# Kernel optimization log

Hardware: AMD Instinct MI355X
Metric: run time of the kernel (lower is better)

## Reference

```python
import jax, jax.numpy as jnp
import numpy as np

B, N, F = 32, 64, 128   # batch, nodes, input features (F == hidden_dim)
E = N * (N - 1)         # fully-connected directed edges = 4032
H, D = 4, 64            # heads, out_dim per head
ALPHA = 0.2             # leaky relu slope


def setup_inputs() -> dict:
    key = jax.random.key(0)
    ks = jax.random.split(key, 16)
    v_self = jax.random.normal(ks[0], (B, N, F), dtype=jnp.float32)
    # fully-connected one-hot sender/receiver matrices [E, N], broadcast to [B, E, N]
    pairs = np.array([(i, j) for i in range(N) for j in range(N) if i != j])
    send = np.zeros((E, N), np.float32); send[np.arange(E), pairs[:, 0]] = 1.0
    rec = np.zeros((E, N), np.float32); rec[np.arange(E), pairs[:, 1]] = 1.0
    rel_send = jnp.broadcast_to(jnp.asarray(send), (B, E, N))
    rel_rec = jnp.broadcast_to(jnp.asarray(rec), (B, E, N))
    s = 0.05
    return {
        "v_self": v_self,
        "rel_rec": rel_rec,
        "rel_send": rel_send,
        "W_proj": jax.random.normal(ks[1], (H * D, F), dtype=jnp.float32) * s,
        "a_fwd": jax.random.normal(ks[2], (H, D), dtype=jnp.float32) * s,
        "a_bwd": jax.random.normal(ks[3], (H, D), dtype=jnp.float32) * s,
        "We1": jax.random.normal(ks[4], (D, 2 * D), dtype=jnp.float32) * s,
        "be1": jnp.zeros((D,), jnp.float32),
        "We2": jax.random.normal(ks[5], (D, D), dtype=jnp.float32) * s,
        "be2": jnp.zeros((D,), jnp.float32),
        "Wv1": jax.random.normal(ks[6], (F, D), dtype=jnp.float32) * s,
        "bv1": jnp.zeros((F,), jnp.float32),
        "Wv2": jax.random.normal(ks[7], (F, F), dtype=jnp.float32) * s,
        "bv2": jnp.zeros((F,), jnp.float32),
        "Wv3": jax.random.normal(ks[8], (D, F), dtype=jnp.float32) * s,
        "bv3": jnp.zeros((D,), jnp.float32),
    }


def _leaky(x):
    return jnp.where(x >= 0, x, ALPHA * x)


def reference(v_self, rel_rec, rel_send, W_proj, a_fwd, a_bwd,
              We1, be1, We2, be2, Wv1, bv1, Wv2, bv2, Wv3, bv3):
    # project: [B,N,F] -> [B,N,H,D]
    v_proj = (v_self @ W_proj.T).reshape(B, N, H, D)
    # gather to edges via one-hot adjacency (v_src==h_src, v_tgt==h_tgt in original)
    h_src = jnp.einsum('ben,bnhd->behd', rel_send, v_proj)
    h_tgt = jnp.einsum('ben,bnhd->behd', rel_rec, v_proj)
    attn_ij = _leaky(jnp.einsum('behd,hd->beh', h_src, a_fwd)) / 500.0
    attn_ji = _leaky(jnp.einsum('behd,hd->beh', h_tgt, a_bwd)) / 500.0
    attn_max = jnp.maximum(attn_ij, attn_ji)
    # NOTE: original applies exp twice (exp of exp); reproduced faithfully
    e_ij = jnp.exp(jnp.exp(attn_ij - attn_max))
    e_ji = jnp.exp(jnp.exp(attn_ji - attn_max))
    alpha_sum = e_ij + e_ji
    alpha_ij = e_ij / alpha_sum   # [B,E,H]
    alpha_ji = e_ji / alpha_sum
    edge_input = jnp.concatenate(
        [alpha_ij[..., None] * h_src, alpha_ji[..., None] * h_tgt], axis=-1)  # [B,E,H,2D]
    # f_CG_e: Linear(2D->D), ReLU, Linear(D->D) on last dim
    e_cg = jax.nn.relu(edge_input @ We1.T + be1) @ We2.T + be2
    edge_weighted = e_cg * alpha_ij[..., None]                               # [B,E,H,D]
    # scatter back to nodes
    v_social = jnp.einsum('behd,ben->bnhd', edge_weighted, rel_rec)          # [B,N,H,D]
    # f_CG_v: Linear(D->F), ReLU, Linear(F->F), ReLU, Linear(F->D)
    x = jax.nn.relu(v_social @ Wv1.T + bv1)
    x = jax.nn.relu(x @ Wv2.T + bv2)
    x = x @ Wv3.T + bv3
    v_out = x.reshape(B, N, H * D)  # concat_heads=True
    return (v_out, alpha_ij)
```

## Files before the change

kernel.cpp:

```cpp
#include <hip/hip_runtime.h>

#define B_ 32
#define N_ 64
#define F_ 128
#define E_ 4032
#define H_ 4
#define D_ 64

typedef __bf16 bf16x8 __attribute__((ext_vector_type(8)));
typedef __bf16 bf16x4 __attribute__((ext_vector_type(4)));
typedef float  f32x4  __attribute__((ext_vector_type(4)));

#define MFMA(a, b, c) __builtin_amdgcn_mfma_f32_16x16x32_bf16(a, b, c, 0, 0, 0)


static __device__ inline bf16x8 ld_cvt8(const float* __restrict__ p) {
    float4 w0 = *(const float4*)p, w1 = *(const float4*)(p + 4);
    bf16x8 b;
    b[0]=(__bf16)w0.x; b[1]=(__bf16)w0.y; b[2]=(__bf16)w0.z; b[3]=(__bf16)w0.w;
    b[4]=(__bf16)w1.x; b[5]=(__bf16)w1.y; b[6]=(__bf16)w1.z; b[7]=(__bf16)w1.w;
    return b;
}

__global__ __launch_bounds__(256) void k_proj(
    const float* __restrict__ v_self, const float* __restrict__ W_proj,
    const float* __restrict__ We1,
    const float* __restrict__ a_fwd, const float* __restrict__ a_bwd,
    const float* __restrict__ Wv1, const float* __restrict__ We2,
    const float* __restrict__ be2, const float* __restrict__ Wv2,
    const float* __restrict__ Wv3,
    float* __restrict__ s_fwd, float* __restrict__ s_bwd,
    __bf16* __restrict__ u_src, __bf16* __restrict__ u_tgt,
    __bf16* __restrict__ M1bf, float* __restrict__ wb,
    __bf16* __restrict__ Wv2bf, __bf16* __restrict__ Wv3bf)
{
    const int t = threadIdx.x;
    const int blk = blockIdx.x;

    if (blk < 32) {
        const int pid = blk * 256 + t;
        const int f = pid >> 6, k = pid & 63;
        float acc = 0.f;
#pragma unroll 8
        for (int dd = 0; dd < 64; ++dd)
            acc += Wv1[f * 64 + dd] * We2[dd * 64 + k];
        M1bf[pid] = (__bf16)acc;
        float p = Wv1[f * 64 + k] * be2[k];
#pragma unroll
        for (int m = 1; m < 64; m <<= 1) p += __shfl_xor(p, m);
        if (k == 0) wb[f] = p;
        Wv2bf[pid]        = (__bf16)Wv2[pid];
        Wv2bf[pid + 8192] = (__bf16)Wv2[pid + 8192];
        Wv3bf[pid]        = (__bf16)Wv3[pid];
        return;
    }

    const int bid = blk - 32;
    const int tile = bid >> 2, w = bid & 3;
    const int node0 = tile * 16;
    const int wsub = t >> 6;
    const int l = t & 63, q = l >> 4, lr = l & 15;

    __shared__ __bf16 P_lds[16 * 72];
    __shared__ float  spart_f[4][16], spart_b[4][16];

    f32x4 acc = {};
#pragma unroll
    for (int ks = 0; ks < 4; ++ks) {
        bf16x8 a = ld_cvt8(v_self + (size_t)(node0 + lr) * 128 + ks * 32 + q * 8);
        bf16x8 bb = ld_cvt8(W_proj + (size_t)(w * 64 + wsub * 16 + lr) * 128 + ks * 32 + q * 8);
        acc = MFMA(a, bb, acc);
    }

    {
        float af = a_fwd[w * 64 + wsub * 16 + lr];
        float ab = a_bwd[w * 64 + wsub * 16 + lr];
        float pf[4], pb[4];
#pragma unroll
        for (int r = 0; r < 4; ++r) { pf[r] = acc[r] * af; pb[r] = acc[r] * ab; }
#pragma unroll
        for (int m = 1; m < 16; m <<= 1)
#pragma unroll
            for (int r = 0; r < 4; ++r) { pf[r] += __shfl_xor(pf[r], m); pb[r] += __shfl_xor(pb[r], m); }
        if (lr == 0) {
#pragma unroll
            for (int r = 0; r < 4; ++r) {
                spart_f[wsub][q * 4 + r] = pf[r];
                spart_b[wsub][q * 4 + r] = pb[r];
            }
        }
#pragma unroll
        for (int r = 0; r < 4; ++r)
            P_lds[(q * 4 + r) * 72 + wsub * 16 + lr] = (__bf16)acc[r];
    }
    __syncthreads();

    if (t < 16) {
        float sf = spart_f[0][t] + spart_f[1][t] + spart_f[2][t] + spart_f[3][t];
        float sb = spart_b[0][t] + spart_b[1][t] + spart_b[2][t] + spart_b[3][t];
        sf = (sf >= 0.f ? sf : 0.2f * sf) * 0.002f;
        sb = (sb >= 0.f ? sb : 0.2f * sb) * 0.002f;
        s_fwd[(node0 + t) * 4 + w] = sf;
        s_bwd[(node0 + t) * 4 + w] = sb;
    }

    const int mm = wsub >> 1, cp = wsub & 1;
    f32x4 uacc[2] = {};
#pragma unroll
    for (int ks = 0; ks < 2; ++ks) {
        bf16x8 a = *(const bf16x8*)&P_lds[lr * 72 + ks * 32 + q * 8];
#pragma unroll
        for (int c = 0; c < 2; ++c) {
            int ct = cp * 2 + c;
            bf16x8 bb = ld_cvt8(We1 + (size_t)(ct * 16 + lr) * 128 + mm * 64 + ks * 32 + q * 8);
            uacc[c] = MFMA(a, bb, uacc[c]);
        }
    }
    __bf16* up = (mm == 0) ? u_src : u_tgt;
#pragma unroll
    for (int c = 0; c < 2; ++c)
#pragma unroll
        for (int r = 0; r < 4; ++r) {
            size_t row = (size_t)(node0 + q * 4 + r) * 4 + w;
            up[row * 64 + (cp * 2 + c) * 16 + lr] = (__bf16)uacc[c][r];
        }
}

__global__ __launch_bounds__(256) void k_fused(
    const float* __restrict__ s_fwd, const float* __restrict__ s_bwd,
    const __bf16* __restrict__ u_src, const __bf16* __restrict__ u_tgt,
    const float* __restrict__ be1,
    const __bf16* __restrict__ M1bf, const float* __restrict__ wb,
    const float* __restrict__ bv1,
    const __bf16* __restrict__ Wv2bf, const float* __restrict__ bv2,
    const __bf16* __restrict__ Wv3bf, const float* __restrict__ bv3,
    float* __restrict__ v_out, float* __restrict__ out_alpha)
{
    const int t = threadIdx.x;
    const int h = t >> 6, d = t & 63;
    const int b = blockIdx.x >> 4, quad = blockIdx.x & 15;
    const int j0 = quad * 4;

    __shared__ __bf16 us_l[64][4][64];
    __shared__ float  ut_l[4][4][64];
    __shared__ float  aij_l[4][64][4];
    __shared__ float  suma_l[16];
    __shared__ __bf16 g_l[16 * 72];
    __shared__ __bf16 X1[16 * 136];
    __shared__ __bf16 X2[16 * 136];

    {
        const __bf16* ub = u_src + (size_t)b * 16384;
        __bf16* dst = &us_l[0][0][0];
#pragma unroll
        for (int it = 0; it < 8; ++it) {
            int idx = it * 2048 + t * 8;
            *(bf16x8*)(dst + idx) = *(const bf16x8*)(ub + idx);
        }
    }
    {
        int idx = t * 4;
        bf16x4 v = *(const bf16x4*)(u_tgt + (size_t)(b * 64 + j0) * 256 + idx);
        int j = idx >> 8, col = idx & 255;
        f32x4 f;
#pragma unroll
        for (int z = 0; z < 4; ++z) f[z] = (float)v[z];
        *(f32x4*)&ut_l[j][col >> 6][col & 63] = f;
    }

    {
        const int i = d;
        float sfi = s_fwd[(b * 64 + i) * 4 + h];
        float areg[4];
#pragma unroll
        for (int jl = 0; jl < 4; ++jl) {
            float sbj = s_bwd[(b * 64 + j0 + jl) * 4 + h];
            float m = fmaxf(sfi, sbj);
            float eij = __expf(__expf(sfi - m));
            float eji = __expf(__expf(sbj - m));
            float aij = eij / (eij + eji);
            if (i == j0 + jl) aij = 0.f;
            areg[jl] = aij;
        }
        f32x4 a4 = {areg[0], areg[1], areg[2], areg[3]};
        *(f32x4*)&aij_l[h][i][0] = a4;
#pragma unroll
        for (int jl = 0; jl < 4; ++jl) {
            float sa = areg[jl];
#pragma unroll
            for (int m2 = 1; m2 < 64; m2 <<= 1) sa += __shfl_xor(sa, m2);
            if (i == 0) suma_l[jl * 4 + h] = sa;
        }
    }
    if (t < 252) {
        const int jj = t >> 2, h2 = t & 3;
#pragma unroll
        for (int s = 0; s < 4; ++s) {
            int i2 = j0 + s;
            int j2 = jj + (jj >= i2 ? 1 : 0);
            float sfi = s_fwd[(b * 64 + i2) * 4 + h2];
            float sbj = s_bwd[(b * 64 + j2) * 4 + h2];
            float m = fmaxf(sfi, sbj);
            float eij = __expf(__expf(sfi - m));
            float eji = __expf(__expf(sbj - m));
            out_alpha[((size_t)b * E_ + i2 * 63 + jj) * 4 + h2] = eij / (eij + eji);
        }
    }
    __syncthreads();

    {
        const float be1d = be1[d];
        float utv[4], utb[4];
#pragma unroll
        for (int jl = 0; jl < 4; ++jl) { utv[jl] = ut_l[jl][h][d]; utb[jl] = utv[jl] + be1d; }
        float gacc[4] = {};
        const __bf16* usp = &us_l[0][h][d];
#pragma unroll 8
        for (int i = 0; i < 64; ++i) {
            float usv = (float)usp[i * 256];
            f32x4 a4 = *(const f32x4*)&aij_l[h][i][0];
#pragma unroll
            for (int jl = 0; jl < 4; ++jl) {
                float a = a4[jl];
                float hp = fmaf(a, usv - utv[jl], utb[jl]);
                gacc[jl] = fmaf(a, fmaxf(hp, 0.f), gacc[jl]);
            }
        }
#pragma unroll
        for (int jl = 0; jl < 4; ++jl)
            g_l[(jl * 4 + h) * 72 + d] = (__bf16)gacc[jl];
    }
    __syncthreads();

    const int w = h;
    const int q = d >> 4, lr = d & 15;

    f32x4 acc1[2] = {};
#pragma unroll
    for (int ks = 0; ks < 2; ++ks) {
        bf16x8 a = *(const bf16x8*)&g_l[lr * 72 + ks * 32 + q * 8];
#pragma unroll
        for (int c = 0; c < 2; ++c) {
            int ct = w * 2 + c;
            bf16x8 bb = *(const bf16x8*)(M1bf + (size_t)(ct * 16 + lr) * 64 + ks * 32 + q * 8);
            acc1[c] = MFMA(a, bb, acc1[c]);
        }
    }
    float sml[4];
#pragma unroll
    for (int r = 0; r < 4; ++r) sml[r] = suma_l[q * 4 + r];
#pragma unroll
    for (int c = 0; c < 2; ++c) {
        int f = (w * 2 + c) * 16 + lr;
        float wbf = wb[f], b1 = bv1[f];
#pragma unroll
        for (int r = 0; r < 4; ++r) {
            float xv = acc1[c][r] + sml[r] * wbf + b1;
            X1[(q * 4 + r) * 136 + f] = (__bf16)fmaxf(xv, 0.f);
        }
    }
    __syncthreads();

    f32x4 acc2[2] = {};
#pragma unroll
    for (int ks = 0; ks < 4; ++ks) {
        bf16x8 a = *(const bf16x8*)&X1[lr * 136 + ks * 32 + q * 8];
#pragma unroll
        for (int c = 0; c < 2; ++c) {
            int ct = w * 2 + c;
            bf16x8 bb = *(const bf16x8*)(Wv2bf + (size_t)(ct * 16 + lr) * 128 + ks * 32 + q * 8);
            acc2[c] = MFMA(a, bb, acc2[c]);
        }
    }
#pragma unroll
    for (int c = 0; c < 2; ++c) {
        int f = (w * 2 + c) * 16 + lr;
        float b2 = bv2[f];
#pragma unroll
        for (int r = 0; r < 4; ++r) {
            float xv = acc2[c][r] + b2;
            X2[(q * 4 + r) * 136 + f] = (__bf16)fmaxf(xv, 0.f);
        }
    }
    __syncthreads();

    f32x4 acc3 = {};
#pragma unroll
    for (int ks = 0; ks < 4; ++ks) {
        bf16x8 a = *(const bf16x8*)&X2[lr * 136 + ks * 32 + q * 8];
        bf16x8 bb = *(const bf16x8*)(Wv3bf + (size_t)(w * 16 + lr) * 128 + ks * 32 + q * 8);
        acc3 = MFMA(a, bb, acc3);
    }
    {
        int dd = w * 16 + lr;
        float b3 = bv3[dd];
        size_t rows_base = (size_t)(b * 64 + j0) * 4;
#pragma unroll
        for (int r = 0; r < 4; ++r)
            v_out[(rows_base + q * 4 + r) * 64 + dd] = acc3[r] + b3;
    }
}

extern "C" void kernel_launch(void* const* d_in, const int* in_sizes, int n_in,
                              void* d_out, int out_size, void* d_ws, size_t ws_size,
                              hipStream_t stream) {
    (void)in_sizes; (void)n_in; (void)out_size; (void)ws_size;
    const float* v_self = (const float*)d_in[0];
    const float* W_proj = (const float*)d_in[3];
    const float* a_fwd  = (const float*)d_in[4];
    const float* a_bwd  = (const float*)d_in[5];
    const float* We1    = (const float*)d_in[6];
    const float* be1    = (const float*)d_in[7];
    const float* We2    = (const float*)d_in[8];
    const float* be2    = (const float*)d_in[9];
    const float* Wv1    = (const float*)d_in[10];
    const float* bv1    = (const float*)d_in[11];
    const float* Wv2    = (const float*)d_in[12];
    const float* bv2    = (const float*)d_in[13];
    const float* Wv3    = (const float*)d_in[14];
    const float* bv3    = (const float*)d_in[15];

    float* ws = (float*)d_ws;
    float*  s_fwd = ws;
    float*  s_bwd = ws + 8192;
    float*  wb    = ws + 24576;
    __bf16* M1bf  = (__bf16*)(ws + 24704);
    __bf16* Wv2bf = (__bf16*)(ws + 28800);
    __bf16* Wv3bf = (__bf16*)(ws + 36992);
    __bf16* u_src = (__bf16*)(ws + 61568);
    __bf16* u_tgt = (__bf16*)(ws + 323712);

    float* v_out = (float*)d_out;
    float* alpha = v_out + (size_t)B_ * N_ * H_ * D_;

    hipLaunchKernelGGL(k_proj, dim3(32 + 512), dim3(256), 0, stream,
                       v_self, W_proj, We1, a_fwd, a_bwd, Wv1, We2, be2, Wv2, Wv3,
                       s_fwd, s_bwd, u_src, u_tgt, M1bf, wb, Wv2bf, Wv3bf);
    hipLaunchKernelGGL(k_fused, dim3(B_ * N_ / 4), dim3(256), 0, stream,
                       s_fwd, s_bwd, u_src, u_tgt, be1, M1bf, wb, bv1,
                       Wv2bf, bv2, Wv3bf, bv3, v_out, alpha);
}
```

Before: 26.53 us.

## Halve per-block receiver nodes and read u_src directly from global memory

Each fused block now handles two receiver nodes instead of four, which doubles the grid to 1024 blocks. The 32KB LDS staging of u_src is dropped, and the edge loop reads the bf16 values straight from global memory, relying on the cache. Half of the 16-row MFMA tile is padding, so the unused g_l rows and suma_l entries are zeroed and the output store is masked. The aim is more parallelism and occupancy. The cost is wasted MFMA work and more global/L2 traffic, since every block rereads u_src.

Result: slower. 29.79 us (+12.3%).

```diff
diff --git a/kernel.cpp b/kernel.cpp
--- a/kernel.cpp
+++ b/kernel.cpp
@@ -10,6 +10,7 @@
 typedef __bf16 bf16x8 __attribute__((ext_vector_type(8)));
 typedef __bf16 bf16x4 __attribute__((ext_vector_type(4)));
 typedef float  f32x4  __attribute__((ext_vector_type(4)));
+typedef float  f32x2  __attribute__((ext_vector_type(2)));
 
 #define MFMA(a, b, c) __builtin_amdgcn_mfma_f32_16x16x32_bf16(a, b, c, 0, 0, 0)
 
@@ -138,42 +139,35 @@
 {
     const int t = threadIdx.x;
     const int h = t >> 6, d = t & 63;
-    const int b = blockIdx.x >> 4, quad = blockIdx.x & 15;
-    const int j0 = quad * 4;
-
-    __shared__ __bf16 us_l[64][4][64];
-    __shared__ float  ut_l[4][4][64];
-    __shared__ float  aij_l[4][64][4];
+    const int b = blockIdx.x >> 5, pr = blockIdx.x & 31;
+    const int j0 = pr * 2;
+
+    __shared__ float  ut_l[2][4][64];
+    __shared__ float  aij_l[4][64][2];
     __shared__ float  suma_l[16];
     __shared__ __bf16 g_l[16 * 72];
     __shared__ __bf16 X1[16 * 136];
     __shared__ __bf16 X2[16 * 136];
 
     {
-        const __bf16* ub = u_src + (size_t)b * 16384;
-        __bf16* dst = &us_l[0][0][0];
-#pragma unroll
-        for (int it = 0; it < 8; ++it) {
-            int idx = it * 2048 + t * 8;
-            *(bf16x8*)(dst + idx) = *(const bf16x8*)(ub + idx);
-        }
-    }
-    {
-        int idx = t * 4;
-        bf16x4 v = *(const bf16x4*)(u_tgt + (size_t)(b * 64 + j0) * 256 + idx);
-        int j = idx >> 8, col = idx & 255;
-        f32x4 f;
-#pragma unroll
-        for (int z = 0; z < 4; ++z) f[z] = (float)v[z];
-        *(f32x4*)&ut_l[j][col >> 6][col & 63] = f;
-    }
+        int idx = t * 2;
+        const __bf16* utp = u_tgt + (size_t)(b * 64 + j0) * 256 + idx;
+        int jl = idx >> 8, col = idx & 255;
+        ut_l[jl][col >> 6][col & 63]             = (float)utp[0];
+        ut_l[jl][(col + 1) >> 6][(col + 1) & 63] = (float)utp[1];
+    }
+    for (int idx = t * 4; idx < 8 * 72; idx += 256 * 4) {
+        bf16x4 z = {};
+        *(bf16x4*)&g_l[8 * 72 + idx] = z;
+    }
+    if (t >= 8 && t < 16) suma_l[t] = 0.f;
 
     {
         const int i = d;
         float sfi = s_fwd[(b * 64 + i) * 4 + h];
-        float areg[4];
-#pragma unroll
-        for (int jl = 0; jl < 4; ++jl) {
+        float areg[2];
+#pragma unroll
+        for (int jl = 0; jl < 2; ++jl) {
             float sbj = s_bwd[(b * 64 + j0 + jl) * 4 + h];
             float m = fmaxf(sfi, sbj);
             float eij = __expf(__expf(sfi - m));
@@ -182,10 +176,10 @@
             if (i == j0 + jl) aij = 0.f;
             areg[jl] = aij;
         }
-        f32x4 a4 = {areg[0], areg[1], areg[2], areg[3]};
-        *(f32x4*)&aij_l[h][i][0] = a4;
-#pragma unroll
-        for (int jl = 0; jl < 4; ++jl) {
+        f32x2 a2 = {areg[0], areg[1]};
+        *(f32x2*)&aij_l[h][i][0] = a2;
+#pragma unroll
+        for (int jl = 0; jl < 2; ++jl) {
             float sa = areg[jl];
 #pragma unroll
             for (int m2 = 1; m2 < 64; m2 <<= 1) sa += __shfl_xor(sa, m2);
@@ -195,7 +189,7 @@
     if (t < 252) {
         const int jj = t >> 2, h2 = t & 3;
 #pragma unroll
-        for (int s = 0; s < 4; ++s) {
+        for (int s = 0; s < 2; ++s) {
             int i2 = j0 + s;
             int j2 = jj + (jj >= i2 ? 1 : 0);
             float sfi = s_fwd[(b * 64 + i2) * 4 + h2];
@@ -210,24 +204,24 @@
 
     {
         const float be1d = be1[d];
-        float utv[4], utb[4];
-#pragma unroll
-        for (int jl = 0; jl < 4; ++jl) { utv[jl] = ut_l[jl][h][d]; utb[jl] = utv[jl] + be1d; }
-        float gacc[4] = {};
-        const __bf16* usp = &us_l[0][h][d];
+        float utv[2], utb[2];
+#pragma unroll
+        for (int jl = 0; jl < 2; ++jl) { utv[jl] = ut_l[jl][h][d]; utb[jl] = utv[jl] + be1d; }
+        float gacc[2] = {};
+        const __bf16* usp = u_src + ((size_t)(b * 64) * 4 + h) * 64 + d;
 #pragma unroll 8
         for (int i = 0; i < 64; ++i) {
             float usv = (float)usp[i * 256];
-            f32x4 a4 = *(const f32x4*)&aij_l[h][i][0];
-#pragma unroll
-            for (int jl = 0; jl < 4; ++jl) {
-                float a = a4[jl];
+            f32x2 a2 = *(const f32x2*)&aij_l[h][i][0];
+#pragma unroll
+            for (int jl = 0; jl < 2; ++jl) {
+                float a = a2[jl];
                 float hp = fmaf(a, usv - utv[jl], utb[jl]);
                 gacc[jl] = fmaf(a, fmaxf(hp, 0.f), gacc[jl]);
             }
         }
 #pragma unroll
-        for (int jl = 0; jl < 4; ++jl)
+        for (int jl = 0; jl < 2; ++jl)
             g_l[(jl * 4 + h) * 72 + d] = (__bf16)gacc[jl];
     }
     __syncthreads();
@@ -291,7 +285,7 @@
         bf16x8 bb = *(const bf16x8*)(Wv3bf + (size_t)(w * 16 + lr) * 128 + ks * 32 + q * 8);
         acc3 = MFMA(a, bb, acc3);
     }
-    {
+    if (q < 2) {
         int dd = w * 16 + lr;
         float b3 = bv3[dd];
         size_t rows_base = (size_t)(b * 64 + j0) * 4;
@@ -336,7 +330,7 @@
     hipLaunchKernelGGL(k_proj, dim3(32 + 512), dim3(256), 0, stream,
                        v_self, W_proj, We1, a_fwd, a_bwd, Wv1, We2, be2, Wv2, Wv3,
                        s_fwd, s_bwd, u_src, u_tgt, M1bf, wb, Wv2bf, Wv3bf);
-    hipLaunchKernelGGL(k_fused, dim3(B_ * N_ / 4), dim3(256), 0, stream,
+    hipLaunchKernelGGL(k_fused, dim3(B_ * N_ / 2), dim3(256), 0, stream,
                        s_fwd, s_bwd, u_src, u_tgt, be1, M1bf, wb, bv1,
                        Wv2bf, bv2, Wv3bf, bv3, v_out, alpha);
 }
```
